# Performance work log

Hardware: AMD Instinct MI355X
Metric: run time of the kernel (lower is better)

Reference implementation:

```python
import jax, jax.numpy as jnp
import numpy as np

B, L, D_MODEL, N_HEADS = 8, 256, 2048, 8
D_HEAD = D_MODEL // N_HEADS  # 256 == L, required by DeltaRuleOperator broadcasting
ALPHA0, BETA0 = 0.1, 0.9      # delta_rule_strength, 1 - strength
LN_EPS = 1e-5


def setup_inputs() -> dict:
    k = jax.random.key(0)
    ks = jax.random.split(k, 8)
    s = 0.02
    return {
        "query": jax.random.normal(ks[0], (B, L, D_MODEL), jnp.float32),
        "key": jax.random.normal(ks[1], (B, L, D_MODEL), jnp.float32),
        "value": jax.random.normal(ks[2], (B, L, D_MODEL), jnp.float32),
        "Wq": jax.random.normal(ks[3], (D_MODEL, D_MODEL), jnp.float32) * s,
        "Wk": jax.random.normal(ks[4], (D_MODEL, D_MODEL), jnp.float32) * s,
        "Wv": jax.random.normal(ks[5], (D_MODEL, D_MODEL), jnp.float32) * s,
        "Wo": jax.random.normal(ks[6], (D_MODEL, D_MODEL), jnp.float32) * s,
        "bo": jnp.zeros((D_MODEL,), jnp.float32),
        "ln_g": jnp.ones((D_MODEL,), jnp.float32),
        "ln_b": jnp.zeros((D_MODEL,), jnp.float32),
        "alpha": jnp.asarray(ALPHA0, jnp.float32),
        "beta": jnp.asarray(BETA0, jnp.float32),
    }


def reference(query, key, value, Wq, Wk, Wv, Wo, bo, ln_g, ln_b, alpha, beta):
    Bs, Ls, D = query.shape
    H, Dh = N_HEADS, D // N_HEADS

    def proj(x, W):  # torch Linear: x @ W.T, split heads -> [B,H,L,Dh]
        return (x @ W.T).reshape(Bs, Ls, H, Dh).transpose(0, 2, 1, 3)

    Q = proj(query, Wq)
    K = proj(key, Wk)
    V = proj(value, Wv)

    # DeltaRuleOperator, applied sequentially per head (buffer mutates across heads)
    kv = jnp.einsum('bhld,bhmd->bhlm', K, V)  # [B,H,L,L] with L == Dh
    kv_heads = jnp.moveaxis(kv, 1, 0)          # [H,B,L,L]

    def cs_step(cs, kv_h):
        # cumulative_state = beta*cs + alpha*detach(mean(kv)); head uses pre-update cs
        new = beta * cs + alpha * jax.lax.stop_gradient(kv_h.mean(axis=(0, 1)))
        return new, cs

    _, cs_seq = jax.lax.scan(cs_step, jnp.zeros((Dh,), query.dtype), kv_heads)  # [H,Dh]
    cs_b = cs_seq[None, :, None, :]                       # [1,H,1,Dh]
    q_mod = Q * (cs_b + alpha * (kv - cs_b))              # delta-rule modulated queries

    # elu feature map
    phi = lambda x: jax.nn.elu(x) + 1.0
    pq, pk = phi(q_mod), phi(K)

    def time_major(x):  # [B,H,L,Dh] -> [L, B*H, Dh]
        return x.reshape(Bs * H, Ls, Dh).transpose(1, 0, 2)

    pq_t, pk_t, v_t = time_major(pq), time_major(pk), time_major(V)

    def step(carry, xs):
        S, Z = carry                        # S:[N,Dh,Dh], Z:[N,Dh]
        q_i, k_i, v_i = xs                  # each [N,Dh]
        S = S + k_i[:, :, None] * v_i[:, None, :]
        Z = Z + k_i
        num = jnp.einsum('nf,nfd->nd', q_i, S)
        den = jnp.maximum(jnp.sum(q_i * Z, axis=-1), 1e-8)
        return (S, Z), num / den[:, None]

    N = Bs * H
    S0 = jnp.zeros((N, Dh, Dh), query.dtype)
    Z0 = jnp.zeros((N, Dh), query.dtype)
    _, outs = jax.lax.scan(step, (S0, Z0), (pq_t, pk_t, v_t))  # [L,N,Dh]

    attn = outs.transpose(1, 0, 2).reshape(Bs, H, Ls, Dh)
    attn = attn.transpose(0, 2, 1, 3).reshape(Bs, Ls, D)       # concat heads

    o = attn @ Wo.T + bo                  # out_proj (dropout is identity in eval)
    x = query + o                          # residual + LayerNorm
    mu = x.mean(-1, keepdims=True)
    var = jnp.mean((x - mu) ** 2, axis=-1, keepdims=True)
    return (x - mu) / jnp.sqrt(var + LN_EPS) * ln_g + ln_b
```

## Files before the change

kernel.cpp:

```cpp
#include <hip/hip_runtime.h>
#include <hip/hip_bf16.h>

using u16 = unsigned short;

typedef __bf16 bf16x8 __attribute__((ext_vector_type(8)));
typedef float  f32x4  __attribute__((ext_vector_type(4)));

typedef __attribute__((address_space(1))) void gas_void;
typedef __attribute__((address_space(3))) void las_void;

__device__ __forceinline__ float b2f(u16 u) {
  union { unsigned u; float f; } v; v.u = ((unsigned)u) << 16; return v.f;
}
__device__ __forceinline__ u16 f2b(float f) {
  union { float f; unsigned u; } v; v.f = f;
  unsigned r = v.u + 0x7fffu + ((v.u >> 16) & 1u);
  return (u16)(r >> 16);
}

__device__ __forceinline__ void gld_lds16(const u16* g, u16* l) {
  __builtin_amdgcn_global_load_lds((gas_void*)g, (las_void*)l, 16, 0, 0);
}

template <int EPI, int BK>
__global__ __launch_bounds__(256) void gemm_bt(
    const u16* __restrict__ A, int lda, long sA1, long sA2,
    const u16* __restrict__ B, int ldb, long sB1, long sB2,
    void* __restrict__ Cv, int ldc, long sC1, long sC2,
    int K, int HDIV,
    const float* __restrict__ bias, const float* __restrict__ resid,
    float* __restrict__ partOut) {
  __shared__ __align__(16) u16 lds[2 * 128 * BK];
  __shared__ float denS[128];
  const int t = threadIdx.x;
  const int lane = t & 63;
  const int wave = t >> 6;
  const int wm = wave >> 1, wn = wave & 1;
  const int laneM = lane & 15, quad = lane >> 4;
  const int zb = blockIdx.z / HDIV, zh = blockIdx.z % HDIV;

  int bx = blockIdx.x, by = blockIdx.y;
  if (EPI == 2) { by = (bx >= 1) ? 1 : 0; bx = (bx == 2) ? 1 : 0; }
  const int kEnd = (EPI == 3) ? ((by + 1) * 128 < K ? (by + 1) * 128 : K) : K;

  const u16* Abase = A + zb * sA1 + zh * sA2 + (long)by * 128 * lda;
  const u16* Bbase = B + zb * sB1 + zh * sB2 + (long)bx * 128 * ldb;

  constexpr int STEPS = BK / 16;
  constexpr int RPS = 2048 / BK;
  constexpr int KK = BK / 32;
  const int sRow = (BK == 64) ? (t >> 3) : (t >> 2);
  const int sg = (BK == 64) ? (t & 7) : (t & 3);
  const int swz = (BK == 64) ? (sg ^ (sRow & 7)) : (sg ^ ((sRow >> 1) & 3));
  const int sc = swz * 8;

  f32x4 acc[4][4];
#pragma unroll
  for (int i = 0; i < 4; ++i)
#pragma unroll
    for (int j = 0; j < 4; ++j) acc[i][j] = (f32x4){0.f, 0.f, 0.f, 0.f};
  float dsum[4] = {0.f, 0.f, 0.f, 0.f};

  for (int k0 = 0; k0 < kEnd; k0 += BK) {
#pragma unroll
    for (int p = 0; p < STEPS; ++p)
      gld_lds16(Abase + (long)(p * RPS + sRow) * lda + k0 + sc,
                &lds[p * 2048 + t * 8]);
#pragma unroll
    for (int p = 0; p < STEPS; ++p)
      gld_lds16(Bbase + (long)(p * RPS + sRow) * ldb + k0 + sc,
                &lds[128 * BK + p * 2048 + t * 8]);
    __syncthreads();
    bf16x8 af[KK][4], bfv[KK][4];
#pragma unroll
    for (int kk = 0; kk < KK; ++kk) {
      int perm8;
      if (BK == 64) perm8 = ((kk * 4 + quad) ^ (laneM & 7)) * 8;
      else          perm8 = (quad ^ ((laneM >> 1) & 3)) * 8;
#pragma unroll
      for (int i = 0; i < 4; ++i) {
        af[kk][i] = *(const bf16x8*)&lds[(wm * 64 + i * 16 + laneM) * BK + perm8];
        bfv[kk][i] =
            *(const bf16x8*)&lds[128 * BK + (wn * 64 + i * 16 + laneM) * BK + perm8];
      }
    }
    if (EPI == 3) {
#pragma unroll
      for (int kk = 0; kk < KK; ++kk)
#pragma unroll
        for (int i = 0; i < 4; ++i) {
          union { bf16x8 v; u16 s[8]; } u; u.v = af[kk][i];
          float ds = 0.f;
#pragma unroll
          for (int e = 0; e < 8; ++e) ds += b2f(u.s[e]);
          dsum[i] += ds;
        }
    }
#pragma unroll
    for (int kk = 0; kk < KK; ++kk)
#pragma unroll
      for (int i = 0; i < 4; ++i)
#pragma unroll
        for (int j = 0; j < 4; ++j)
          acc[i][j] = __builtin_amdgcn_mfma_f32_16x16x32_bf16(
              af[kk][i], bfv[kk][j], acc[i][j], 0, 0, 0);
    __syncthreads();
  }

  if (EPI == 3) {
#pragma unroll
    for (int i = 0; i < 4; ++i) {
      float s = dsum[i];
      s += __shfl_xor(s, 16);
      s += __shfl_xor(s, 32);
      if (wn == 0 && quad == 0)
        denS[wm * 64 + i * 16 + laneM] = fmaxf(s, 1e-8f);
    }
    __syncthreads();
  }

  if (EPI == 1) {
#pragma unroll
    for (int j = 0; j < 4; ++j) {
      float s = 0.f;
#pragma unroll
      for (int i = 0; i < 4; ++i)
#pragma unroll
        for (int r = 0; r < 4; ++r) s += acc[i][j][r];
      s += __shfl_xor(s, 16);
      s += __shfl_xor(s, 32);
      if (quad == 0)
        atomicAdd(&partOut[zh * 256 + bx * 128 + wn * 64 + j * 16 + laneM], s);
    }
  }

  const long cOff = zb * sC1 + zh * sC2;
  const int colB = bx * 128 + wn * 64;
#pragma unroll
  for (int i = 0; i < 4; ++i) {
#pragma unroll
    for (int j = 0; j < 4; ++j) {
#pragma unroll
      for (int r = 0; r < 4; ++r) {
        const int lrow = wm * 64 + i * 16 + quad * 4 + r;
        const int row = by * 128 + lrow;
        const int col = colB + j * 16 + laneM;
        const long idx = cOff + (long)row * ldc + col;
        float v = acc[i][j][r];
        if (EPI == 0 || EPI == 1) {
          ((u16*)Cv)[idx] = f2b(v);
        } else if (EPI == 2) {
          ((u16*)Cv)[idx] = f2b(col <= row ? v : 0.0f);
        } else if (EPI == 3) {
          ((u16*)Cv)[idx] = f2b(v / denS[lrow]);
        } else {
          ((float*)Cv)[idx] =
              (zb == 0) ? v + bias[col] + resid[(long)row * ldc + col] : v;
        }
      }
    }
  }
}

__device__ __forceinline__ void g256_tile(
    const u16* __restrict__ la, const u16* __restrict__ lb,
    u16* __restrict__ sa, u16* __restrict__ sb, int tau, int nt,
    const u16* AgR0, const u16* AgR1, const u16* BgR0, const u16* BgR1,
    int rowA, int rowB, int rg, int t, f32x4 (&acc)[8][4]) {
  const bool st = (tau + 3) < nt;
  const int ks = (tau + 3) << 5;
  bf16x8 af[4], bv[4];
#pragma unroll
  for (int m = 0; m < 4; ++m)
    af[m] = *(const bf16x8*)&la[(rowA + m * 16) * 32 + rg];
#pragma unroll
  for (int n = 0; n < 4; ++n)
    bv[n] = *(const bf16x8*)&lb[(rowB + n * 16) * 32 + rg];
  if (st) {
    gld_lds16(AgR0 + ks, &sa[t * 8]);
    gld_lds16(AgR1 + ks, &sa[4096 + t * 8]);
  }
  __builtin_amdgcn_s_barrier();
  asm volatile("s_waitcnt lgkmcnt(0)" ::: "memory");
  __builtin_amdgcn_s_setprio(1);
#pragma unroll
  for (int m = 0; m < 4; ++m)
#pragma unroll
    for (int n = 0; n < 4; ++n)
      acc[m][n] = __builtin_amdgcn_mfma_f32_16x16x32_bf16(af[m], bv[n],
                                                          acc[m][n], 0, 0, 0);
  __builtin_amdgcn_s_setprio(0);
  __builtin_amdgcn_s_barrier();
#pragma unroll
  for (int m = 0; m < 4; ++m)
    af[m] = *(const bf16x8*)&la[(rowA + 64 + m * 16) * 32 + rg];
  if (st) {
    gld_lds16(BgR0 + ks, &sb[t * 8]);
    gld_lds16(BgR1 + ks, &sb[4096 + t * 8]);
  }
  __builtin_amdgcn_s_barrier();
  asm volatile("s_waitcnt lgkmcnt(0)" ::: "memory");
  __builtin_amdgcn_s_setprio(1);
#pragma unroll
  for (int m = 0; m < 4; ++m)
#pragma unroll
    for (int n = 0; n < 4; ++n)
      acc[4 + m][n] = __builtin_amdgcn_mfma_f32_16x16x32_bf16(
          af[m], bv[n], acc[4 + m][n], 0, 0, 0);
  __builtin_amdgcn_s_setprio(0);
  if (tau < nt - 1) {
    if (tau + 3 < nt)
      asm volatile("s_waitcnt vmcnt(8)" ::: "memory");
    else if (tau + 2 < nt)
      asm volatile("s_waitcnt vmcnt(4)" ::: "memory");
    else
      asm volatile("s_waitcnt vmcnt(0)" ::: "memory");
    __builtin_amdgcn_s_barrier();
  }
}

template <int EPI>
__global__ __launch_bounds__(512) void gemm256(
    const u16* __restrict__ A, int lda, long sA1,
    const u16* __restrict__ B, int ldb, long sB1,
    void* __restrict__ Cv, int ldc, long sC1, int K,
    const float* __restrict__ bias, const float* __restrict__ resid) {
  __shared__ __align__(16) u16 A0[8192], A1[8192], A2[8192], A3[8192];
  __shared__ __align__(16) u16 B0[8192], B1[8192], B2[8192], B3[8192];
  const int t = threadIdx.x;
  const int lane = t & 63, wave = t >> 6;
  const int wm = wave >> 2, wn = wave & 3;
  const int laneM = lane & 15, quad = lane >> 4;

  const int cpx = gridDim.x >> 3;
  const int id2 = (blockIdx.x & 7) * cpx + (blockIdx.x >> 3);
  const int bx = id2 & 7, by = (id2 >> 3) & 7, z = id2 >> 6;

  const u16* Ag = A + (long)z * sA1 + (long)by * 256 * lda;
  const u16* Bg = B + (long)z * sB1 + (long)bx * 256 * ldb;

  const int nt = K >> 5;
  const int rg = (quad ^ ((laneM >> 1) & 3)) * 8;
  const int rowA = wm * 128 + laneM;
  const int rowB = wn * 64 + laneM;

  const int sRow0 = t >> 2, sRow1 = (512 + t) >> 2;
  const int sc0 = (((t) & 3) ^ ((sRow0 >> 1) & 3)) * 8;
  const int sc1 = (((512 + t) & 3) ^ ((sRow1 >> 1) & 3)) * 8;
  const u16* AgR0 = Ag + (long)sRow0 * lda + sc0;
  const u16* AgR1 = Ag + (long)sRow1 * lda + sc1;
  const u16* BgR0 = Bg + (long)sRow0 * ldb + sc0;
  const u16* BgR1 = Bg + (long)sRow1 * ldb + sc1;

  f32x4 acc[8][4];
#pragma unroll
  for (int i = 0; i < 8; ++i)
#pragma unroll
    for (int j = 0; j < 4; ++j) acc[i][j] = (f32x4){0.f, 0.f, 0.f, 0.f};

  gld_lds16(AgR0, &A0[t * 8]);      gld_lds16(AgR1, &A0[4096 + t * 8]);
  gld_lds16(BgR0, &B0[t * 8]);      gld_lds16(BgR1, &B0[4096 + t * 8]);
  gld_lds16(AgR0 + 32, &A1[t * 8]); gld_lds16(AgR1 + 32, &A1[4096 + t * 8]);
  gld_lds16(BgR0 + 32, &B1[t * 8]); gld_lds16(BgR1 + 32, &B1[4096 + t * 8]);
  gld_lds16(AgR0 + 64, &A2[t * 8]); gld_lds16(AgR1 + 64, &A2[4096 + t * 8]);
  gld_lds16(BgR0 + 64, &B2[t * 8]); gld_lds16(BgR1 + 64, &B2[4096 + t * 8]);
  asm volatile("s_waitcnt vmcnt(8)" ::: "memory");
  __builtin_amdgcn_s_barrier();

  for (int tau = 0; tau < nt; tau += 4) {
    g256_tile(A0, B0, A3, B3, tau, nt, AgR0, AgR1, BgR0, BgR1, rowA, rowB,
              rg, t, acc);
    g256_tile(A1, B1, A0, B0, tau + 1, nt, AgR0, AgR1, BgR0, BgR1, rowA,
              rowB, rg, t, acc);
    g256_tile(A2, B2, A1, B1, tau + 2, nt, AgR0, AgR1, BgR0, BgR1, rowA,
              rowB, rg, t, acc);
    g256_tile(A3, B3, A2, B2, tau + 3, nt, AgR0, AgR1, BgR0, BgR1, rowA,
              rowB, rg, t, acc);
  }

  const long cOff = (long)z * sC1;
  const int colB = bx * 256 + wn * 64;
  const int rowBase = by * 256 + wm * 128;
#pragma unroll
  for (int i = 0; i < 8; ++i) {
#pragma unroll
    for (int j = 0; j < 4; ++j) {
#pragma unroll
      for (int r = 0; r < 4; ++r) {
        const int row = rowBase + i * 16 + quad * 4 + r;
        const int col = colB + j * 16 + laneM;
        const long idx = cOff + (long)row * ldc + col;
        float v = acc[i][j][r];
        if (EPI == 0) {
          ((u16*)Cv)[idx] = f2b(v);
        } else {
          ((float*)Cv)[idx] =
              (z == 0) ? v + bias[col] + resid[(long)row * ldc + col] : v;
        }
      }
    }
  }
}

__global__ __launch_bounds__(512) void fused_av(
    const u16* __restrict__ pq, const u16* __restrict__ pk,
    const u16* __restrict__ Vt, u16* __restrict__ attnb) {
  __shared__ __align__(16) u16 PQ[64 * 256];
  __shared__ __align__(16) u16 PK[64 * 256];
  __shared__ __align__(16) u16 VT0[256 * 64];
  __shared__ __align__(16) u16 VT1[256 * 64];
  __shared__ __align__(16) u16 SL[64 * 72];
  __shared__ float denS[64];
  const int t = threadIdx.x;
  const int lane = t & 63, wave = t >> 6;
  const int wm = wave >> 2, wn = wave & 3;
  const int laneM = lane & 15, quad = lane >> 4;
  const int by = blockIdx.x, z = blockIdx.z;
  const int nj = by + 1;
  const long zo = (long)z * 65536;

  const u16* pqg = pq + zo + (long)by * 64 * 256;
  const u16* pkg = pk + zo;
  const u16* vtg = Vt + zo;

#pragma unroll
  for (int p = 0; p < 4; ++p) {
    int c = p * 512 + t, r = c >> 5, g = c & 31;
    gld_lds16(pqg + r * 256 + ((g ^ (r & 7)) * 8), &PQ[c * 8]);
  }
#pragma unroll
  for (int p = 0; p < 4; ++p) {
    int c = p * 512 + t, r = c >> 5, g = c & 31;
    gld_lds16(pkg + r * 256 + ((g ^ (r & 7)) * 8), &PK[c * 8]);
  }
#pragma unroll
  for (int p = 0; p < 4; ++p) {
    int c = p * 512 + t, r = c >> 3, g = c & 7;
    gld_lds16(vtg + r * 256 + ((g ^ (r & 7)) * 8), &VT0[c * 8]);
  }
  asm volatile("s_waitcnt vmcnt(0)" ::: "memory");
  __builtin_amdgcn_s_barrier();

  f32x4 acc[2][4];
#pragma unroll
  for (int i = 0; i < 2; ++i)
#pragma unroll
    for (int j = 0; j < 4; ++j) acc[i][j] = (f32x4){0.f, 0.f, 0.f, 0.f};
  float dsum[2] = {0.f, 0.f};

  for (int jt = 0; jt < nj; ++jt) {
    const u16* VT = (jt & 1) ? VT1 : VT0;
    u16* VTn = (jt & 1) ? VT0 : VT1;
    f32x4 s0 = (f32x4){0.f, 0.f, 0.f, 0.f};
    f32x4 s1 = (f32x4){0.f, 0.f, 0.f, 0.f};
#pragma unroll
    for (int kk = 0; kk < 8; ++kk) {
      const int pg = ((kk * 4 + quad) ^ (laneM & 7)) * 8;
      bf16x8 bk = *(const bf16x8*)&PK[(wn * 16 + laneM) * 256 + pg];
      bf16x8 a0 = *(const bf16x8*)&PQ[(wm * 32 + laneM) * 256 + pg];
      bf16x8 a1 = *(const bf16x8*)&PQ[(wm * 32 + 16 + laneM) * 256 + pg];
      s0 = __builtin_amdgcn_mfma_f32_16x16x32_bf16(a0, bk, s0, 0, 0, 0);
      s1 = __builtin_amdgcn_mfma_f32_16x16x32_bf16(a1, bk, s1, 0, 0, 0);
    }
    {
      const int jcol = jt * 64 + wn * 16 + laneM;
#pragma unroll
      for (int r = 0; r < 4; ++r) {
        int l0 = wm * 32 + quad * 4 + r;
        int l1 = l0 + 16;
        SL[l0 * 72 + wn * 16 + laneM] =
            f2b(jcol <= by * 64 + l0 ? s0[r] : 0.f);
        SL[l1 * 72 + wn * 16 + laneM] =
            f2b(jcol <= by * 64 + l1 ? s1[r] : 0.f);
      }
    }
    __builtin_amdgcn_s_barrier();
    const bool st = (jt + 1) < nj;
    if (st) {
#pragma unroll
      for (int p = 0; p < 4; ++p) {
        int c = p * 512 + t, r = c >> 5, g = c & 31;
        gld_lds16(pkg + ((jt + 1) * 64 + r) * 256 + ((g ^ (r & 7)) * 8),
                  &PK[c * 8]);
      }
#pragma unroll
      for (int p = 0; p < 4; ++p) {
        int c = p * 512 + t, r = c >> 3, g = c & 7;
        gld_lds16(vtg + r * 256 + (jt + 1) * 64 + ((g ^ (r & 7)) * 8),
                  &VTn[c * 8]);
      }
    }
#pragma unroll
    for (int kk = 0; kk < 2; ++kk) {
#pragma unroll
      for (int i = 0; i < 2; ++i) {
        bf16x8 sa = *(const bf16x8*)&SL[(wm * 32 + i * 16 + laneM) * 72 +
                                        kk * 32 + quad * 8];
        union { bf16x8 v; u16 s[8]; } u; u.v = sa;
        float ds = 0.f;
#pragma unroll
        for (int e = 0; e < 8; ++e) ds += b2f(u.s[e]);
        dsum[i] += ds;
#pragma unroll
        for (int jj = 0; jj < 4; ++jj) {
          const int drow = wn * 64 + jj * 16 + laneM;
          bf16x8 vb = *(const bf16x8*)&VT[drow * 64 +
                                          (((kk * 4 + quad) ^ (laneM & 7)) * 8)];
          acc[i][jj] =
              __builtin_amdgcn_mfma_f32_16x16x32_bf16(sa, vb, acc[i][jj], 0, 0, 0);
        }
      }
    }
    if (st) asm volatile("s_waitcnt vmcnt(0)" ::: "memory");
    __builtin_amdgcn_s_barrier();
  }

#pragma unroll
  for (int i = 0; i < 2; ++i) {
    float s = dsum[i];
    s += __shfl_xor(s, 16);
    s += __shfl_xor(s, 32);
    if (wn == 0 && quad == 0)
      denS[wm * 32 + i * 16 + laneM] = fmaxf(s, 1e-8f);
  }
  __builtin_amdgcn_s_barrier();

  const long obase =
      ((long)(z >> 3) * 256 + by * 64) * 2048 + (z & 7) * 256;
#pragma unroll
  for (int i = 0; i < 2; ++i) {
#pragma unroll
    for (int jj = 0; jj < 4; ++jj) {
#pragma unroll
      for (int r = 0; r < 4; ++r) {
        const int lrow = wm * 32 + i * 16 + quad * 4 + r;
        const int d = wn * 64 + jj * 16 + laneM;
        attnb[obase + (long)lrow * 2048 + d] = f2b(acc[i][jj][r] / denS[lrow]);
      }
    }
  }
}

__global__ __launch_bounds__(256) void convert7(
    const float* __restrict__ s0, const float* __restrict__ s1,
    const float* __restrict__ s2, const float* __restrict__ s3,
    const float* __restrict__ s4, const float* __restrict__ s5,
    const float* __restrict__ s6, u16* __restrict__ dst) {
  long idx = (long)blockIdx.x * 256 + threadIdx.x;
  int seg = (int)(idx >> 20);
  long off = (idx & 1048575) << 2;
  const float* s;
  switch (seg) {
    case 0: s = s0; break; case 1: s = s1; break; case 2: s = s2; break;
    case 3: s = s3; break; case 4: s = s4; break; case 5: s = s5; break;
    default: s = s6;
  }
  float4 v = *(const float4*)(s + off);
  ushort4 o;
  o.x = f2b(v.x); o.y = f2b(v.y); o.z = f2b(v.z); o.w = f2b(v.w);
  *(ushort4*)(dst + (long)seg * 4194304 + off) = o;
}

__global__ __launch_bounds__(256) void pqpk_kernel(
    const u16* __restrict__ Qp, const u16* __restrict__ Kp,
    const u16* __restrict__ kv, const float* __restrict__ part,
    const float* __restrict__ alphaP, const float* __restrict__ betaP,
    u16* __restrict__ pq, u16* __restrict__ pk) {
  long base = ((long)blockIdx.x * 256 + threadIdx.x) * 8;
  int d0 = (int)(base & 255), h = (int)((base >> 16) & 7);
  float alpha = *alphaP, beta = *betaP;
  float cf[8] = {0.f, 0.f, 0.f, 0.f, 0.f, 0.f, 0.f, 0.f};
  for (int hh = 0; hh < h; ++hh) {
    float4 p0 = *(const float4*)(part + hh * 256 + d0);
    float4 p1 = *(const float4*)(part + hh * 256 + d0 + 4);
    const float sc = alpha * (1.0f / 2048.0f);
    cf[0] = beta * cf[0] + sc * p0.x;
    cf[1] = beta * cf[1] + sc * p0.y;
    cf[2] = beta * cf[2] + sc * p0.z;
    cf[3] = beta * cf[3] + sc * p0.w;
    cf[4] = beta * cf[4] + sc * p1.x;
    cf[5] = beta * cf[5] + sc * p1.y;
    cf[6] = beta * cf[6] + sc * p1.z;
    cf[7] = beta * cf[7] + sc * p1.w;
  }
  long pidx = ((long)((int)(base >> 19) * 256 + (int)((base >> 8) & 255))) * 2048 +
              h * 256 + d0;
  ushort4 q0 = *(const ushort4*)(Qp + pidx);
  ushort4 q1 = *(const ushort4*)(Qp + pidx + 4);
  ushort4 k0 = *(const ushort4*)(Kp + pidx);
  ushort4 k1 = *(const ushort4*)(Kp + pidx + 4);
  ushort4 v0 = *(const ushort4*)(kv + base);
  ushort4 v1 = *(const ushort4*)(kv + base + 4);
  u16 qs[8] = {q0.x, q0.y, q0.z, q0.w, q1.x, q1.y, q1.z, q1.w};
  u16 ks[8] = {k0.x, k0.y, k0.z, k0.w, k1.x, k1.y, k1.z, k1.w};
  u16 vs[8] = {v0.x, v0.y, v0.z, v0.w, v1.x, v1.y, v1.z, v1.w};
  u16 oq[8], ok[8];
#pragma unroll
  for (int e = 0; e < 8; ++e) {
    float qm = b2f(qs[e]) * (cf[e] + alpha * (b2f(vs[e]) - cf[e]));
    oq[e] = f2b(qm > 0.f ? qm + 1.f : expf(qm));
    float Kv = b2f(ks[e]);
    ok[e] = f2b(Kv > 0.f ? Kv + 1.f : expf(Kv));
  }
  *(ushort4*)(pq + base) = (ushort4){oq[0], oq[1], oq[2], oq[3]};
  *(ushort4*)(pq + base + 4) = (ushort4){oq[4], oq[5], oq[6], oq[7]};
  *(ushort4*)(pk + base) = (ushort4){ok[0], ok[1], ok[2], ok[3]};
  *(ushort4*)(pk + base + 4) = (ushort4){ok[4], ok[5], ok[6], ok[7]};
}

__global__ __launch_bounds__(256) void vtrans_kernel(const u16* __restrict__ Vp,
                                                     u16* __restrict__ Vt) {
  __shared__ u16 tile[32][33];
  int z = blockIdx.z, b = z >> 3, h = z & 7;
  int jT = blockIdx.x * 32, dT = blockIdx.y * 32;
  int tx = threadIdx.x, ty = threadIdx.y;
#pragma unroll
  for (int ii = 0; ii < 4; ++ii) {
    int j = jT + ty + ii * 8, d = dT + tx;
    tile[ty + ii * 8][tx] = Vp[(long)(b * 256 + j) * 2048 + h * 256 + d];
  }
  __syncthreads();
#pragma unroll
  for (int ii = 0; ii < 4; ++ii) {
    int d = dT + ty + ii * 8, j = jT + tx;
    Vt[(long)z * 65536 + d * 256 + j] = tile[tx][ty + ii * 8];
  }
}

__global__ __launch_bounds__(256) void ln_kernel(
    const float* __restrict__ x0, const float* __restrict__ x1,
    const float* __restrict__ g, const float* __restrict__ bb,
    float* __restrict__ out) {
  int row = blockIdx.x, t = threadIdx.x;
  const float4* xr0 = (const float4*)(x0 + (long)row * 2048);
  const float4* xr1 = (const float4*)(x1 + (long)row * 2048);
  float4 a0 = xr0[t], b0 = xr1[t], a1 = xr0[t + 256], b1 = xr1[t + 256];
  float4 v0, v1;
  v0.x = a0.x + b0.x; v0.y = a0.y + b0.y; v0.z = a0.z + b0.z; v0.w = a0.w + b0.w;
  v1.x = a1.x + b1.x; v1.y = a1.y + b1.y; v1.z = a1.z + b1.z; v1.w = a1.w + b1.w;
  float s = v0.x + v0.y + v0.z + v0.w + v1.x + v1.y + v1.z + v1.w;
  float ss = v0.x * v0.x + v0.y * v0.y + v0.z * v0.z + v0.w * v0.w +
             v1.x * v1.x + v1.y * v1.y + v1.z * v1.z + v1.w * v1.w;
  for (int o = 32; o; o >>= 1) { s += __shfl_xor(s, o); ss += __shfl_xor(ss, o); }
  __shared__ float a1s[4], a2s[4];
  int wave = t >> 6, lane = t & 63;
  if (lane == 0) { a1s[wave] = s; a2s[wave] = ss; }
  __syncthreads();
  s = a1s[0] + a1s[1] + a1s[2] + a1s[3];
  ss = a2s[0] + a2s[1] + a2s[2] + a2s[3];
  float mu = s * (1.f / 2048.f);
  float var = ss * (1.f / 2048.f) - mu * mu;
  float rstd = rsqrtf(var + 1e-5f);
  const float4* g4 = (const float4*)g;
  const float4* b4 = (const float4*)bb;
  float4* orow = (float4*)(out + (long)row * 2048);
  float4 gg = g4[t], bv = b4[t], r;
  r.x = (v0.x - mu) * rstd * gg.x + bv.x;
  r.y = (v0.y - mu) * rstd * gg.y + bv.y;
  r.z = (v0.z - mu) * rstd * gg.z + bv.z;
  r.w = (v0.w - mu) * rstd * gg.w + bv.w;
  orow[t] = r;
  gg = g4[t + 256]; bv = b4[t + 256];
  r.x = (v1.x - mu) * rstd * gg.x + bv.x;
  r.y = (v1.y - mu) * rstd * gg.y + bv.y;
  r.z = (v1.z - mu) * rstd * gg.z + bv.z;
  r.w = (v1.w - mu) * rstd * gg.w + bv.w;
  orow[t + 256] = r;
}

extern "C" void kernel_launch(void* const* d_in, const int* in_sizes, int n_in,
                              void* d_out, int out_size, void* d_ws,
                              size_t ws_size, hipStream_t stream) {
  const float* query = (const float*)d_in[0];
  const float* key = (const float*)d_in[1];
  const float* value = (const float*)d_in[2];
  const float* Wq = (const float*)d_in[3];
  const float* Wk = (const float*)d_in[4];
  const float* Wv = (const float*)d_in[5];
  const float* Wo = (const float*)d_in[6];
  const float* bo = (const float*)d_in[7];
  const float* ln_g = (const float*)d_in[8];
  const float* ln_b = (const float*)d_in[9];
  const float* alphaP = (const float*)d_in[10];
  const float* betaP = (const float*)d_in[11];

  char* ws = (char*)d_ws;
  const long SZ = 8388608;
  u16* qb = (u16*)(ws);
  u16* Wb = (u16*)(ws + 3 * SZ);
  u16* Qp = (u16*)(ws + 7 * SZ);
  u16* kvb = (u16*)(ws + 10 * SZ);
  u16* pq = (u16*)(ws + 12 * SZ);
  u16* pk = (u16*)(ws + 13 * SZ);
  u16* Vt = (u16*)(ws + 14 * SZ);
  u16* attnb = (u16*)(ws + 15 * SZ);
  float* x0 = (float*)(ws + 12 * SZ);
  float* x1 = (float*)(ws);
  float* part = (float*)(ws + 16 * SZ);

  u16* Kp = Qp + 4194304;
  u16* Vp = Qp + 8388608;
  u16* Wob = Wb + 3 * 4194304;

  hipMemsetAsync(part, 0, 8 * 256 * sizeof(float), stream);

  convert7<<<28672, 256, 0, stream>>>(query, key, value, Wq, Wk, Wv, Wo, qb);

  gemm256<0><<<dim3(192, 1, 1), 512, 0, stream>>>(
      qb, 2048, 4194304L, Wb, 2048, 4194304L, (void*)Qp, 2048, 4194304L,
      2048, nullptr, nullptr);

  gemm_bt<1, 64><<<dim3(2, 2, 64), 256, 0, stream>>>(
      Kp, 2048, 524288L, 256L, Vp, 2048, 524288L, 256L, (void*)kvb, 256,
      524288L, 65536L, 256, 8, nullptr, nullptr, part);

  pqpk_kernel<<<2048, 256, 0, stream>>>(Qp, Kp, kvb, part, alphaP, betaP,
                                        pq, pk);

  vtrans_kernel<<<dim3(8, 8, 64), dim3(32, 8), 0, stream>>>(Vp, Vt);

  fused_av<<<dim3(4, 1, 64), 512, 0, stream>>>(pq, pk, Vt, attnb);

  gemm256<4><<<dim3(128, 1, 1), 512, 0, stream>>>(
      attnb, 2048, 1024L, Wob, 2048, 1024L, (void*)x0, 2048, -25165824L,
      1024, bo, query);

  ln_kernel<<<2048, 256, 0, stream>>>(x0, x1, ln_g, ln_b, (float*)d_out);
}
```

Measured before the change: 334.1 us.

## Fold memset into convert, merge V transpose into pqpk, swap out-proj GEMM

Removes the separate memset by having extra blocks of the convert kernel zero the partial-sum buffer. Merges the V transpose into the pqpk kernel as extra blocks, using a wider 64x64 tile with 16-byte vector loads and stores. Replaces the gemm256 output projection with the generic gemm_bt kernel using BK=32 over a 16x16x2 split-K grid, and drops unused EPI 2/3 paths. The aim is fewer launches and better occupancy for the out-projection, at the cost of a possibly less efficient GEMM tile and LDS bank conflicts in the transpose reads.

```diff
diff --git a/kernel.cpp b/kernel.cpp
--- a/kernel.cpp
+++ b/kernel.cpp
@@ -5,6 +5,7 @@
 
 typedef __bf16 bf16x8 __attribute__((ext_vector_type(8)));
 typedef float  f32x4  __attribute__((ext_vector_type(4)));
+typedef u16    u16x8  __attribute__((ext_vector_type(8)));
 
 typedef __attribute__((address_space(1))) void gas_void;
 typedef __attribute__((address_space(3))) void las_void;
@@ -40,8 +41,7 @@
   const int zb = blockIdx.z / HDIV, zh = blockIdx.z % HDIV;
 
   int bx = blockIdx.x, by = blockIdx.y;
-  if (EPI == 2) { by = (bx >= 1) ? 1 : 0; bx = (bx == 2) ? 1 : 0; }
-  const int kEnd = (EPI == 3) ? ((by + 1) * 128 < K ? (by + 1) * 128 : K) : K;
+  const int kEnd = K;
 
   const u16* Abase = A + zb * sA1 + zh * sA2 + (long)by * 128 * lda;
   const u16* Bbase = B + zb * sB1 + zh * sB2 + (long)bx * 128 * ldb;
@@ -59,7 +59,6 @@
   for (int i = 0; i < 4; ++i)
 #pragma unroll
     for (int j = 0; j < 4; ++j) acc[i][j] = (f32x4){0.f, 0.f, 0.f, 0.f};
-  float dsum[4] = {0.f, 0.f, 0.f, 0.f};
 
   for (int k0 = 0; k0 < kEnd; k0 += BK) {
 #pragma unroll
@@ -84,18 +83,6 @@
             *(const bf16x8*)&lds[128 * BK + (wn * 64 + i * 16 + laneM) * BK + perm8];
       }
     }
-    if (EPI == 3) {
-#pragma unroll
-      for (int kk = 0; kk < KK; ++kk)
-#pragma unroll
-        for (int i = 0; i < 4; ++i) {
-          union { bf16x8 v; u16 s[8]; } u; u.v = af[kk][i];
-          float ds = 0.f;
-#pragma unroll
-          for (int e = 0; e < 8; ++e) ds += b2f(u.s[e]);
-          dsum[i] += ds;
-        }
-    }
 #pragma unroll
     for (int kk = 0; kk < KK; ++kk)
 #pragma unroll
@@ -106,18 +93,7 @@
               af[kk][i], bfv[kk][j], acc[i][j], 0, 0, 0);
     __syncthreads();
   }
-
-  if (EPI == 3) {
-#pragma unroll
-    for (int i = 0; i < 4; ++i) {
-      float s = dsum[i];
-      s += __shfl_xor(s, 16);
-      s += __shfl_xor(s, 32);
-      if (wn == 0 && quad == 0)
-        denS[wm * 64 + i * 16 + laneM] = fmaxf(s, 1e-8f);
-    }
-    __syncthreads();
-  }
+  (void)denS;
 
   if (EPI == 1) {
 #pragma unroll
@@ -149,10 +125,6 @@
         float v = acc[i][j][r];
         if (EPI == 0 || EPI == 1) {
           ((u16*)Cv)[idx] = f2b(v);
-        } else if (EPI == 2) {
-          ((u16*)Cv)[idx] = f2b(col <= row ? v : 0.0f);
-        } else if (EPI == 3) {
-          ((u16*)Cv)[idx] = f2b(v / denS[lrow]);
         } else {
           ((float*)Cv)[idx] =
               (zb == 0) ? v + bias[col] + resid[(long)row * ldc + col] : v;
@@ -445,7 +417,13 @@
     const float* __restrict__ s0, const float* __restrict__ s1,
     const float* __restrict__ s2, const float* __restrict__ s3,
     const float* __restrict__ s4, const float* __restrict__ s5,
-    const float* __restrict__ s6, u16* __restrict__ dst) {
+    const float* __restrict__ s6, u16* __restrict__ dst,
+    float* __restrict__ part) {
+  if (blockIdx.x >= 28672) {
+    int m = (blockIdx.x - 28672) * 256 + threadIdx.x;
+    if (m < 2048) part[m] = 0.f;
+    return;
+  }
   long idx = (long)blockIdx.x * 256 + threadIdx.x;
   int seg = (int)(idx >> 20);
   long off = (idx & 1048575) << 2;
@@ -461,12 +439,38 @@
   *(ushort4*)(dst + (long)seg * 4194304 + off) = o;
 }
 
-__global__ __launch_bounds__(256) void pqpk_kernel(
+__global__ __launch_bounds__(256) void pqpk_vt_kernel(
     const u16* __restrict__ Qp, const u16* __restrict__ Kp,
     const u16* __restrict__ kv, const float* __restrict__ part,
     const float* __restrict__ alphaP, const float* __restrict__ betaP,
-    u16* __restrict__ pq, u16* __restrict__ pk) {
-  long base = ((long)blockIdx.x * 256 + threadIdx.x) * 8;
+    u16* __restrict__ pq, u16* __restrict__ pk,
+    const u16* __restrict__ Vp, u16* __restrict__ Vt) {
+  __shared__ __align__(16) u16 tile[64][72];
+  const int t = threadIdx.x;
+  const int bid = blockIdx.x;
+  if (bid >= 2048) {
+    const int vt = bid - 2048;
+    const int z = vt >> 4, rem = vt & 15;
+    const int jT = (rem & 3) * 64, dT = (rem >> 2) * 64;
+    const int b = z >> 3, h = z & 7;
+    const int jr = t >> 2, ds = (t & 3) * 16;
+    const u16* src = Vp + (long)(b * 256 + jT + jr) * 2048 + h * 256 + dT + ds;
+    *(u16x8*)&tile[jr][ds] = *(const u16x8*)src;
+    *(u16x8*)&tile[jr][ds + 8] = *(const u16x8*)(src + 8);
+    __syncthreads();
+    const int dr = t >> 2, js = (t & 3) * 16;
+    union { u16x8 v; u16 s[8]; } o0, o1;
+#pragma unroll
+    for (int k = 0; k < 8; ++k) {
+      o0.s[k] = tile[js + k][dr];
+      o1.s[k] = tile[js + 8 + k][dr];
+    }
+    u16* dstp = Vt + (long)z * 65536 + (long)(dT + dr) * 256 + jT + js;
+    *(u16x8*)dstp = o0.v;
+    *(u16x8*)(dstp + 8) = o1.v;
+    return;
+  }
+  long base = ((long)bid * 256 + t) * 8;
   int d0 = (int)(base & 255), h = (int)((base >> 16) & 7);
   float alpha = *alphaP, beta = *betaP;
   float cf[8] = {0.f, 0.f, 0.f, 0.f, 0.f, 0.f, 0.f, 0.f};
@@ -506,25 +510,6 @@
   *(ushort4*)(pq + base + 4) = (ushort4){oq[4], oq[5], oq[6], oq[7]};
   *(ushort4*)(pk + base) = (ushort4){ok[0], ok[1], ok[2], ok[3]};
   *(ushort4*)(pk + base + 4) = (ushort4){ok[4], ok[5], ok[6], ok[7]};
-}
-
-__global__ __launch_bounds__(256) void vtrans_kernel(const u16* __restrict__ Vp,
-                                                     u16* __restrict__ Vt) {
-  __shared__ u16 tile[32][33];
-  int z = blockIdx.z, b = z >> 3, h = z & 7;
-  int jT = blockIdx.x * 32, dT = blockIdx.y * 32;
-  int tx = threadIdx.x, ty = threadIdx.y;
-#pragma unroll
-  for (int ii = 0; ii < 4; ++ii) {
-    int j = jT + ty + ii * 8, d = dT + tx;
-    tile[ty + ii * 8][tx] = Vp[(long)(b * 256 + j) * 2048 + h * 256 + d];
-  }
-  __syncthreads();
-#pragma unroll
-  for (int ii = 0; ii < 4; ++ii) {
-    int d = dT + ty + ii * 8, j = jT + tx;
-    Vt[(long)z * 65536 + d * 256 + j] = tile[tx][ty + ii * 8];
-  }
 }
 
 __global__ __launch_bounds__(256) void ln_kernel(
@@ -602,9 +587,8 @@
   u16* Vp = Qp + 8388608;
   u16* Wob = Wb + 3 * 4194304;
 
-  hipMemsetAsync(part, 0, 8 * 256 * sizeof(float), stream);
-
-  convert7<<<28672, 256, 0, stream>>>(query, key, value, Wq, Wk, Wv, Wo, qb);
+  convert7<<<28680, 256, 0, stream>>>(query, key, value, Wq, Wk, Wv, Wo, qb,
+                                      part);
 
   gemm256<0><<<dim3(192, 1, 1), 512, 0, stream>>>(
       qb, 2048, 4194304L, Wb, 2048, 4194304L, (void*)Qp, 2048, 4194304L,
@@ -614,16 +598,14 @@
       Kp, 2048, 524288L, 256L, Vp, 2048, 524288L, 256L, (void*)kvb, 256,
       524288L, 65536L, 256, 8, nullptr, nullptr, part);
 
-  pqpk_kernel<<<2048, 256, 0, stream>>>(Qp, Kp, kvb, part, alphaP, betaP,
-                                        pq, pk);
-
-  vtrans_kernel<<<dim3(8, 8, 64), dim3(32, 8), 0, stream>>>(Vp, Vt);
+  pqpk_vt_kernel<<<3072, 256, 0, stream>>>(Qp, Kp, kvb, part, alphaP, betaP,
+                                           pq, pk, Vp, Vt);
 
   fused_av<<<dim3(4, 1, 64), 512, 0, stream>>>(pq, pk, Vt, attnb);
 
-  gemm256<4><<<dim3(128, 1, 1), 512, 0, stream>>>(
-      attnb, 2048, 1024L, Wob, 2048, 1024L, (void*)x0, 2048, -25165824L,
-      1024, bo, query);
+  gemm_bt<4, 32><<<dim3(16, 16, 2), 256, 0, stream>>>(
+      attnb, 2048, 1024L, 0L, Wob, 2048, 1024L, 0L, (void*)x0, 2048,
+      -25165824L, 0L, 1024, 1, bo, query, nullptr);
 
   ln_kernel<<<2048, 256, 0, stream>>>(x0, x1, ln_g, ln_b, (float*)d_out);
 }
```

Result: faster. 313.6 us (-6.1%).
